# Kernel tuning notes

Hardware: AMD Instinct MI355X
Metric: run time of the kernel (lower is better)

Reference implementation:

```python
import jax, jax.numpy as jnp
import numpy as np
from jax import lax

B, C_IN, C_OUT, H, W, E = 16, 256, 256, 32, 32, 8


def setup_inputs() -> dict:
    key = jax.random.key(0)
    k = jax.random.split(key, 5)
    x = jax.random.normal(k[0], (B, C_IN, H, W), dtype=jnp.float32)
    # router: Conv2d(C_IN, E, kernel_size=1) -> weight [E, C_IN], bias [E]
    wc = jax.random.normal(k[1], (E, C_IN), dtype=jnp.float32) / np.sqrt(C_IN)
    bc = jnp.zeros((E,), dtype=jnp.float32)
    # experts: E x Conv2d(C_IN, C_OUT, 3, padding=1) + ReLU
    we = jax.random.normal(k[2], (E, C_OUT, C_IN, 3, 3), dtype=jnp.float32) / np.sqrt(C_IN * 9)
    be = jnp.zeros((E, C_OUT), dtype=jnp.float32)
    return {"x": x, "wc": wc, "bc": bc, "we": we, "be": be}


def reference(x, wc, bc, we, be):
    Bx = x.shape[0]
    # controller: 1x1 conv then global avg-pool == pool then linear
    pooled = jnp.mean(x, axis=(2, 3))                      # [B, C_IN]
    logits = pooled @ wc.T + bc                            # [B, E]
    decisions = jnp.argmax(logits, axis=1)                 # [B] int
    # run ALL experts on the full batch as one grouped conv: weight [E*C_OUT, C_IN, 3, 3]
    w_all = we.reshape(E * C_OUT, C_IN, 3, 3)
    y = lax.conv_general_dilated(
        x, w_all, window_strides=(1, 1), padding="SAME",
        dimension_numbers=("NCHW", "OIHW", "NCHW"))        # [B, E*C_OUT, H, W]
    y = y + be.reshape(1, E * C_OUT, 1, 1)
    y = jax.nn.relu(y).reshape(Bx, E, C_OUT, H, W)
    # faithful to forward_test: out block i is components[dec[i]](x) for the FULL batch
    # out[i*B + j] = y[j, dec[i]]
    gathered = y[:, decisions]                             # [j, i, C_OUT, H, W]
    out = jnp.swapaxes(gathered, 0, 1).reshape(Bx * Bx, C_OUT, H, W)
    return out
```

## Files before the change

### kernel.cpp

```cpp
#include <hip/hip_runtime.h>
#include <hip/hip_bf16.h>
#include <stdint.h>

#define B_    16
#define CIN   256
#define COUT  256
#define E_    8
#define HW    1024
#define PH    34
#define PW    34

typedef __attribute__((ext_vector_type(8))) short  short8;
typedef __attribute__((ext_vector_type(4))) float  floatx4;

#define XT_OFF 17408
#define XT_BYTES (B_*PH*PW*CIN*2)
#define WT_OFF (XT_OFF + XT_BYTES)

__device__ __forceinline__ void gld_lds16(const void* g, void* l) {
    __builtin_amdgcn_global_load_lds(
        (const __attribute__((address_space(1))) unsigned int*)g,
        (__attribute__((address_space(3))) unsigned int*)l,
        16, 0, 0);
}

__global__ void pool_kernel(const float* __restrict__ x, float* __restrict__ pooled) {
    int b = blockIdx.x, c = blockIdx.y;
    const float4* p = (const float4*)(x + ((size_t)b*CIN + c)*HW);
    int t = threadIdx.x;
    float4 v = p[t];
    float s = v.x + v.y + v.z + v.w;
    #pragma unroll
    for (int o = 32; o > 0; o >>= 1) s += __shfl_down(s, o, 64);
    __shared__ float wsum[4];
    if ((t & 63) == 0) wsum[t >> 6] = s;
    __syncthreads();
    if (t == 0) pooled[b*CIN + c] = (wsum[0]+wsum[1]+wsum[2]+wsum[3]) * (1.0f/1024.0f);
}

__global__ void decide_kernel(const float* __restrict__ pooled, const float* __restrict__ wc,
                              const float* __restrict__ bc, int* __restrict__ dec) {
    int t = threadIdx.x;
    int b = t >> 3, e = t & 7;
    float acc = bc[e];
    const float4* pp = (const float4*)(pooled + b*CIN);
    const float4* ww = (const float4*)(wc + e*CIN);
    #pragma unroll 4
    for (int i = 0; i < CIN/4; ++i) {
        float4 p = pp[i], w = ww[i];
        acc += p.x*w.x + p.y*w.y + p.z*w.z + p.w*w.w;
    }
    __shared__ float lg[16][8];
    lg[b][e] = acc;
    __syncthreads();
    if (e == 0) {
        float best = lg[b][0]; int bi = 0;
        #pragma unroll
        for (int j = 1; j < 8; ++j) { if (lg[b][j] > best) { best = lg[b][j]; bi = j; } }
        dec[b] = bi;
    }
}

__global__ void xpose_kernel(const float* __restrict__ x, unsigned short* __restrict__ xt) {
    int b = blockIdx.x;
    int hw0 = blockIdx.y * 32;
    int ci0 = blockIdx.z * 32;
    __shared__ float tile[32][33];
    int t = threadIdx.x;
    int j = t & 31;
    int i = t >> 5;
    #pragma unroll
    for (int p = 0; p < 4; ++p)
        tile[i + p*8][j] = x[((size_t)b*CIN + ci0 + i + p*8)*HW + hw0 + j];
    __syncthreads();
    if (t < 128) {
        int g = t & 3;
        int hwl = t >> 2;
        int hw = hw0 + hwl;
        int h = hw >> 5, w = hw & 31;
        short8 v;
        #pragma unroll
        for (int q = 0; q < 8; ++q) {
            __hip_bfloat16 hv = __float2bfloat16(tile[g*8 + q][hwl]);
            v[q] = *(short*)&hv;
        }
        *(short8*)&xt[(((size_t)b*PH + h + 1)*PW + (w + 1))*CIN + ci0 + g*8] = v;
    }
}

__global__ void wpose_kernel(const float* __restrict__ we, unsigned short* __restrict__ wt) {
    int e = blockIdx.x >> 8, co = blockIdx.x & 255;
    __shared__ float buf[CIN*9];
    const float* src = we + ((size_t)e*COUT + co)*CIN*9;
    int t = threadIdx.x;
    #pragma unroll
    for (int k = 0; k < 9; ++k) buf[t + k*256] = src[t + k*256];
    __syncthreads();
    for (int idx = t; idx < 288; idx += 256) {
        int rs = idx >> 5, grp = idx & 31;
        short8 v;
        #pragma unroll
        for (int q = 0; q < 8; ++q) {
            __hip_bfloat16 h = __float2bfloat16(buf[(grp*8 + q)*9 + rs]);
            v[q] = *(short*)&h;
        }
        *(short8*)&wt[(((size_t)e*9 + rs)*COUT + co)*CIN + grp*8] = v;
    }
}

__global__ __launch_bounds__(256) void conv_kernel(
    const unsigned short* __restrict__ xt, const unsigned short* __restrict__ wt,
    const float* __restrict__ be, const int* __restrict__ dec,
    float* __restrict__ out) {

    int tile = blockIdx.x;
    int b = blockIdx.y;
    int e = blockIdx.z;
    int mt = tile >> 3, nt = tile & 7;

    int dcs[16];
    #pragma unroll
    for (int i = 0; i < 16; ++i) dcs[i] = dec[i];
    bool active = false;
    #pragma unroll
    for (int i = 0; i < 16; ++i) active |= (dcs[i] == e);
    if (!active) return;

    __shared__ __align__(16) unsigned short sA[3][512*8];
    __shared__ __align__(16) unsigned short sB[2][832*8];

    int t = threadIdx.x;
    int wave = t >> 6, lane = t & 63;
    int wm = wave >> 1, wn = wave & 1;
    int kg = lane >> 4, ln = lane & 15;

    int ph0 = nt * 4;
    int co0 = mt * 128;

    floatx4 acc[4][4];
    #pragma unroll
    for (int i = 0; i < 4; ++i)
        #pragma unroll
        for (int j = 0; j < 4; ++j) acc[i][j] = (floatx4)0.0f;

    const unsigned short* xb = xt + ((size_t)b*PH + ph0)*PW*CIN;
    const unsigned short* wb = wt + (size_t)e*9*COUT*CIN + (size_t)co0*CIN;

    auto stageA = [&](int ck, int sh, int buf) {
        const unsigned short* wsrc = wb + (size_t)sh*COUT*CIN + ck*32;
        #pragma unroll
        for (int k = 0; k < 2; ++k) {
            int c = t + k*256;
            int row = c >> 2, gs = c & 3;
            int g = gs ^ ((row >> 1) & 3);
            gld_lds16(wsrc + (size_t)row*CIN + g*8, &sA[buf][c*8]);
        }
    };
    auto stageB = [&](int ck, int buf) {
        const unsigned short* xsrc = xb + ck*32;
        #pragma unroll
        for (int k = 0; k < 3; ++k) {
            int c = t + k*256;
            int rB = c >> 2, gs = c & 3;
            int g = gs ^ ((rB >> 1) & 3);
            gld_lds16(xsrc + (size_t)rB*CIN + g*8, &sB[buf][c*8]);
        }
        if (t < 64) {
            int c = t + 768;
            int cc = c < 816 ? c : 815;
            int rB = cc >> 2, gs = cc & 3;
            int g = gs ^ ((rB >> 1) & 3);
            gld_lds16(xsrc + (size_t)rB*CIN + g*8, &sB[buf][c*8]);
        }
    };

    stageB(0, 0);
    stageA(0, 0, 0);
    stageA(0, 1, 1);
    asm volatile("s_waitcnt vmcnt(2)" ::: "memory");
    __builtin_amdgcn_s_barrier();

    for (int ck = 0; ck < 8; ++ck) {
        int bb_ = ck & 1;
        for (int sh = 0; sh < 9; ++sh) {
            int it = ck*9 + sh;
            int ab = it % 3;

            int nit = it + 2;
            bool doA = (nit < 72);
            if (doA) {
                int nck = nit / 9;
                stageA(nck, nit - nck*9, nit % 3);
            }
            bool doB = (sh == 7) && (ck < 7);
            if (doB) stageB(ck + 1, bb_ ^ 1);

            short8 a[4], bv[4];
            #pragma unroll
            for (int im = 0; im < 4; ++im) {
                int row = wm*64 + im*16 + ln;
                int cL = row*4 + (kg ^ ((row >> 1) & 3));
                a[im] = *(const short8*)(&sA[ab][cL*8]);
            }
            int r = sh / 3, s = sh - r*3;
            #pragma unroll
            for (int in = 0; in < 4; ++in) {
                int n  = wn*64 + in*16 + ln;
                int hl = n >> 5, wl = n & 31;
                int rB = (hl + r)*34 + (wl + s);
                int cL = rB*4 + (kg ^ ((rB >> 1) & 3));
                bv[in] = *(const short8*)(&sB[bb_][cL*8]);
            }

            #pragma unroll
            for (int im = 0; im < 4; ++im)
                #pragma unroll
                for (int in = 0; in < 4; ++in)
                    acc[im][in] = __builtin_amdgcn_mfma_f32_16x16x32_bf16(bv[in], a[im], acc[im][in], 0, 0, 0);

            if (doA) {
                if (doB) {
                    if (wave == 0) asm volatile("s_waitcnt vmcnt(6) lgkmcnt(0)" ::: "memory");
                    else           asm volatile("s_waitcnt vmcnt(5) lgkmcnt(0)" ::: "memory");
                } else {
                    asm volatile("s_waitcnt vmcnt(2) lgkmcnt(0)" ::: "memory");
                }
            } else {
                asm volatile("s_waitcnt vmcnt(0) lgkmcnt(0)" ::: "memory");
            }
            __builtin_amdgcn_s_barrier();
        }
    }

    float bias[4];
    #pragma unroll
    for (int im = 0; im < 4; ++im)
        bias[im] = be[e*COUT + co0 + wm*64 + im*16 + ln];
    #pragma unroll
    for (int im = 0; im < 4; ++im)
        #pragma unroll
        for (int in = 0; in < 4; ++in)
            #pragma unroll
            for (int rg = 0; rg < 4; ++rg) {
                float v = acc[im][in][rg] + bias[im];
                acc[im][in][rg] = v > 0.0f ? v : 0.0f;
            }

    for (int i = 0; i < 16; ++i) {
        if (dcs[i] != e) continue;
        float* ob = out + (size_t)(i*16 + b)*COUT*HW;
        #pragma unroll
        for (int im = 0; im < 4; ++im) {
            int co = co0 + wm*64 + im*16 + ln;
            float* orow = ob + (size_t)co*HW + nt*128 + wn*64 + kg*4;
            #pragma unroll
            for (int in = 0; in < 4; ++in)
                *(floatx4*)(orow + in*16) = acc[im][in];
        }
    }
}

extern "C" void kernel_launch(void* const* d_in, const int* in_sizes, int n_in,
                              void* d_out, int out_size, void* d_ws, size_t ws_size,
                              hipStream_t stream) {
    const float* x  = (const float*)d_in[0];
    const float* wc = (const float*)d_in[1];
    const float* bc = (const float*)d_in[2];
    const float* we = (const float*)d_in[3];
    const float* be = (const float*)d_in[4];
    float* out = (float*)d_out;

    char* ws = (char*)d_ws;
    int*   dec    = (int*)ws;
    float* pooled = (float*)(ws + 64);
    unsigned short* xt = (unsigned short*)(ws + XT_OFF);
    unsigned short* wt = (unsigned short*)(ws + WT_OFF);

    hipMemsetAsync(xt, 0, XT_BYTES, stream);

    pool_kernel  <<<dim3(16, 256), 256, 0, stream>>>(x, pooled);
    decide_kernel<<<1, 128, 0, stream>>>(pooled, wc, bc, dec);
    xpose_kernel <<<dim3(16, 32, 8), 256, 0, stream>>>(x, xt);
    wpose_kernel <<<2048, 256, 0, stream>>>(we, wt);
    conv_kernel  <<<dim3(16, 16, 8), 256, 0, stream>>>(xt, wt, be, dec, out);
}
```

Measured before the change: 453.6 us.

## Fuse pooling into transpose and single-buffer conv input tile for occupancy

Folds the global average pool into the input transpose kernel with per-tile sums accumulated through atomicAdd, which removes a separate pass over x. The 1/1024 scale moves into the decision kernel, and the memset now also zeroes the pooled buffer. The conv kernel drops the double-buffered input tile to a single buffer, reloading it after a barrier at the last shift of each channel chunk, and adds a launch bound of 4 blocks per CU. The aim is to cut LDS use and raise occupancy, at the cost of an extra barrier and load stall once per chunk.

```diff
diff --git a/kernel.cpp b/kernel.cpp
--- a/kernel.cpp
+++ b/kernel.cpp
@@ -24,25 +24,45 @@
         16, 0, 0);
 }
 
-__global__ void pool_kernel(const float* __restrict__ x, float* __restrict__ pooled) {
-    int b = blockIdx.x, c = blockIdx.y;
-    const float4* p = (const float4*)(x + ((size_t)b*CIN + c)*HW);
-    int t = threadIdx.x;
-    float4 v = p[t];
-    float s = v.x + v.y + v.z + v.w;
-    #pragma unroll
-    for (int o = 32; o > 0; o >>= 1) s += __shfl_down(s, o, 64);
-    __shared__ float wsum[4];
-    if ((t & 63) == 0) wsum[t >> 6] = s;
+__global__ void xpose_kernel(const float* __restrict__ x, unsigned short* __restrict__ xt,
+                             float* __restrict__ pooled) {
+    int b = blockIdx.x;
+    int hw0 = blockIdx.y * 32;
+    int ci0 = blockIdx.z * 32;
+    __shared__ float tile[32][33];
+    int t = threadIdx.x;
+    int j = t & 31;
+    int i = t >> 5;
+    #pragma unroll
+    for (int p = 0; p < 4; ++p)
+        tile[i + p*8][j] = x[((size_t)b*CIN + ci0 + i + p*8)*HW + hw0 + j];
     __syncthreads();
-    if (t == 0) pooled[b*CIN + c] = (wsum[0]+wsum[1]+wsum[2]+wsum[3]) * (1.0f/1024.0f);
+    if (t < 32) {
+        float s = 0.0f;
+        #pragma unroll
+        for (int q = 0; q < 32; ++q) s += tile[t][q];
+        atomicAdd(&pooled[b*CIN + ci0 + t], s);
+    }
+    if (t < 128) {
+        int g = t & 3;
+        int hwl = t >> 2;
+        int hw = hw0 + hwl;
+        int h = hw >> 5, w = hw & 31;
+        short8 v;
+        #pragma unroll
+        for (int q = 0; q < 8; ++q) {
+            __hip_bfloat16 hv = __float2bfloat16(tile[g*8 + q][hwl]);
+            v[q] = *(short*)&hv;
+        }
+        *(short8*)&xt[(((size_t)b*PH + h + 1)*PW + (w + 1))*CIN + ci0 + g*8] = v;
+    }
 }
 
 __global__ void decide_kernel(const float* __restrict__ pooled, const float* __restrict__ wc,
                               const float* __restrict__ bc, int* __restrict__ dec) {
     int t = threadIdx.x;
     int b = t >> 3, e = t & 7;
-    float acc = bc[e];
+    float acc = 0.0f;
     const float4* pp = (const float4*)(pooled + b*CIN);
     const float4* ww = (const float4*)(wc + e*CIN);
     #pragma unroll 4
@@ -50,6 +70,7 @@
         float4 p = pp[i], w = ww[i];
         acc += p.x*w.x + p.y*w.y + p.z*w.z + p.w*w.w;
     }
+    acc = acc * (1.0f/1024.0f) + bc[e];
     __shared__ float lg[16][8];
     lg[b][e] = acc;
     __syncthreads();
@@ -61,33 +82,6 @@
     }
 }
 
-__global__ void xpose_kernel(const float* __restrict__ x, unsigned short* __restrict__ xt) {
-    int b = blockIdx.x;
-    int hw0 = blockIdx.y * 32;
-    int ci0 = blockIdx.z * 32;
-    __shared__ float tile[32][33];
-    int t = threadIdx.x;
-    int j = t & 31;
-    int i = t >> 5;
-    #pragma unroll
-    for (int p = 0; p < 4; ++p)
-        tile[i + p*8][j] = x[((size_t)b*CIN + ci0 + i + p*8)*HW + hw0 + j];
-    __syncthreads();
-    if (t < 128) {
-        int g = t & 3;
-        int hwl = t >> 2;
-        int hw = hw0 + hwl;
-        int h = hw >> 5, w = hw & 31;
-        short8 v;
-        #pragma unroll
-        for (int q = 0; q < 8; ++q) {
-            __hip_bfloat16 hv = __float2bfloat16(tile[g*8 + q][hwl]);
-            v[q] = *(short*)&hv;
-        }
-        *(short8*)&xt[(((size_t)b*PH + h + 1)*PW + (w + 1))*CIN + ci0 + g*8] = v;
-    }
-}
-
 __global__ void wpose_kernel(const float* __restrict__ we, unsigned short* __restrict__ wt) {
     int e = blockIdx.x >> 8, co = blockIdx.x & 255;
     __shared__ float buf[CIN*9];
@@ -108,7 +102,7 @@
     }
 }
 
-__global__ __launch_bounds__(256) void conv_kernel(
+__global__ __launch_bounds__(256, 4) void conv_kernel(
     const unsigned short* __restrict__ xt, const unsigned short* __restrict__ wt,
     const float* __restrict__ be, const int* __restrict__ dec,
     float* __restrict__ out) {
@@ -127,7 +121,7 @@
     if (!active) return;
 
     __shared__ __align__(16) unsigned short sA[3][512*8];
-    __shared__ __align__(16) unsigned short sB[2][832*8];
+    __shared__ __align__(16) unsigned short sB[816*8];
 
     int t = threadIdx.x;
     int wave = t >> 6, lane = t & 63;
@@ -156,60 +150,69 @@
             gld_lds16(wsrc + (size_t)row*CIN + g*8, &sA[buf][c*8]);
         }
     };
-    auto stageB = [&](int ck, int buf) {
+    auto stageB = [&](int ck) {
         const unsigned short* xsrc = xb + ck*32;
         #pragma unroll
         for (int k = 0; k < 3; ++k) {
             int c = t + k*256;
             int rB = c >> 2, gs = c & 3;
             int g = gs ^ ((rB >> 1) & 3);
-            gld_lds16(xsrc + (size_t)rB*CIN + g*8, &sB[buf][c*8]);
+            gld_lds16(xsrc + (size_t)rB*CIN + g*8, &sB[c*8]);
         }
         if (t < 64) {
             int c = t + 768;
             int cc = c < 816 ? c : 815;
             int rB = cc >> 2, gs = cc & 3;
             int g = gs ^ ((rB >> 1) & 3);
-            gld_lds16(xsrc + (size_t)rB*CIN + g*8, &sB[buf][c*8]);
+            if (c < 816) gld_lds16(xsrc + (size_t)rB*CIN + g*8, &sB[c*8]);
+            else         gld_lds16(xsrc + (size_t)rB*CIN + g*8, &sB[815*8]);
         }
     };
 
-    stageB(0, 0);
+    stageB(0);
     stageA(0, 0, 0);
     stageA(0, 1, 1);
     asm volatile("s_waitcnt vmcnt(2)" ::: "memory");
     __builtin_amdgcn_s_barrier();
 
     for (int ck = 0; ck < 8; ++ck) {
-        int bb_ = ck & 1;
         for (int sh = 0; sh < 9; ++sh) {
             int it = ck*9 + sh;
             int ab = it % 3;
-
-            int nit = it + 2;
-            bool doA = (nit < 72);
-            if (doA) {
-                int nck = nit / 9;
-                stageA(nck, nit - nck*9, nit % 3);
-            }
-            bool doB = (sh == 7) && (ck < 7);
-            if (doB) stageB(ck + 1, bb_ ^ 1);
+            int r = sh / 3, s = sh - r*3;
+            bool doA = (it + 2 < 72);
 
             short8 a[4], bv[4];
-            #pragma unroll
-            for (int im = 0; im < 4; ++im) {
-                int row = wm*64 + im*16 + ln;
-                int cL = row*4 + (kg ^ ((row >> 1) & 3));
-                a[im] = *(const short8*)(&sA[ab][cL*8]);
-            }
-            int r = sh / 3, s = sh - r*3;
-            #pragma unroll
-            for (int in = 0; in < 4; ++in) {
-                int n  = wn*64 + in*16 + ln;
-                int hl = n >> 5, wl = n & 31;
-                int rB = (hl + r)*34 + (wl + s);
-                int cL = rB*4 + (kg ^ ((rB >> 1) & 3));
-                bv[in] = *(const short8*)(&sB[bb_][cL*8]);
+            auto readA = [&]() {
+                #pragma unroll
+                for (int im = 0; im < 4; ++im) {
+                    int row = wm*64 + im*16 + ln;
+                    int cL = row*4 + (kg ^ ((row >> 1) & 3));
+                    a[im] = *(const short8*)(&sA[ab][cL*8]);
+                }
+            };
+            auto readB = [&]() {
+                #pragma unroll
+                for (int in = 0; in < 4; ++in) {
+                    int n  = wn*64 + in*16 + ln;
+                    int hl = n >> 5, wl = n & 31;
+                    int rB = (hl + r)*34 + (wl + s);
+                    int cL = rB*4 + (kg ^ ((rB >> 1) & 3));
+                    bv[in] = *(const short8*)(&sB[cL*8]);
+                }
+            };
+
+            if (sh == 8 && ck < 7) {
+                readB();
+                asm volatile("s_waitcnt lgkmcnt(0)" ::: "memory");
+                __builtin_amdgcn_s_barrier();
+                stageB(ck + 1);
+                { int nit = it + 2; int nck = nit/9; stageA(nck, nit - nck*9, nit % 3); }
+                readA();
+            } else {
+                if (doA) { int nit = it + 2; int nck = nit/9; stageA(nck, nit - nck*9, nit % 3); }
+                readA();
+                readB();
             }
 
             #pragma unroll
@@ -218,17 +221,11 @@
                 for (int in = 0; in < 4; ++in)
                     acc[im][in] = __builtin_amdgcn_mfma_f32_16x16x32_bf16(bv[in], a[im], acc[im][in], 0, 0, 0);
 
-            if (doA) {
-                if (doB) {
-                    if (wave == 0) asm volatile("s_waitcnt vmcnt(6) lgkmcnt(0)" ::: "memory");
-                    else           asm volatile("s_waitcnt vmcnt(5) lgkmcnt(0)" ::: "memory");
-                } else {
-                    asm volatile("s_waitcnt vmcnt(2) lgkmcnt(0)" ::: "memory");
-                }
-            } else {
-                asm volatile("s_waitcnt vmcnt(0) lgkmcnt(0)" ::: "memory");
+            if (it != 71) {
+                if (doA) asm volatile("s_waitcnt vmcnt(2) lgkmcnt(0)" ::: "memory");
+                else     asm volatile("s_waitcnt vmcnt(0) lgkmcnt(0)" ::: "memory");
+                __builtin_amdgcn_s_barrier();
             }
-            __builtin_amdgcn_s_barrier();
         }
     }
 
@@ -276,11 +273,10 @@
     unsigned short* xt = (unsigned short*)(ws + XT_OFF);
     unsigned short* wt = (unsigned short*)(ws + WT_OFF);
 
-    hipMemsetAsync(xt, 0, XT_BYTES, stream);
-
-    pool_kernel  <<<dim3(16, 256), 256, 0, stream>>>(x, pooled);
+    hipMemsetAsync(ws, 0, XT_OFF + XT_BYTES, stream);
+
+    xpose_kernel <<<dim3(16, 32, 8), 256, 0, stream>>>(x, xt, pooled);
+    wpose_kernel <<<2048, 256, 0, stream>>>(we, wt);
     decide_kernel<<<1, 128, 0, stream>>>(pooled, wc, bc, dec);
-    xpose_kernel <<<dim3(16, 32, 8), 256, 0, stream>>>(x, xt);
-    wpose_kernel <<<2048, 256, 0, stream>>>(we, wt);
     conv_kernel  <<<dim3(16, 16, 8), 256, 0, stream>>>(xt, wt, be, dec, out);
 }
```

Result: slower. 491.4 us (+8.3%).

## Fuse prep kernels, compute routing inside conv, simplify pipeline to double buffering

Applied to the files above, without the earlier changes.

Merges pooling, activation transpose, border zeroing and weight transpose into one prep kernel, which removes the full-tensor memset and several launches. Each conv block now recomputes the router logits and argmax from the pooled sums, so the separate decide kernel goes away. The conv main loop drops the triple-buffered A pipeline with hand-tuned vmcnt waits in favour of plain double buffering with __syncthreads, which may expose more load latency. sB grows to 1024 rows, so LDS use per block rises.

```diff
diff --git a/kernel.cpp b/kernel.cpp
--- a/kernel.cpp
+++ b/kernel.cpp
@@ -24,112 +24,122 @@
         16, 0, 0);
 }
 
-__global__ void pool_kernel(const float* __restrict__ x, float* __restrict__ pooled) {
-    int b = blockIdx.x, c = blockIdx.y;
-    const float4* p = (const float4*)(x + ((size_t)b*CIN + c)*HW);
+__global__ void prep_kernel(const float* __restrict__ x, const float* __restrict__ we,
+                            unsigned short* __restrict__ xt, unsigned short* __restrict__ wt,
+                            float* __restrict__ pooled) {
+    int bid = blockIdx.x;
     int t = threadIdx.x;
-    float4 v = p[t];
-    float s = v.x + v.y + v.z + v.w;
-    #pragma unroll
-    for (int o = 32; o > 0; o >>= 1) s += __shfl_down(s, o, 64);
-    __shared__ float wsum[4];
-    if ((t & 63) == 0) wsum[t >> 6] = s;
-    __syncthreads();
-    if (t == 0) pooled[b*CIN + c] = (wsum[0]+wsum[1]+wsum[2]+wsum[3]) * (1.0f/1024.0f);
-}
-
-__global__ void decide_kernel(const float* __restrict__ pooled, const float* __restrict__ wc,
-                              const float* __restrict__ bc, int* __restrict__ dec) {
-    int t = threadIdx.x;
-    int b = t >> 3, e = t & 7;
-    float acc = bc[e];
-    const float4* pp = (const float4*)(pooled + b*CIN);
-    const float4* ww = (const float4*)(wc + e*CIN);
-    #pragma unroll 4
-    for (int i = 0; i < CIN/4; ++i) {
-        float4 p = pp[i], w = ww[i];
-        acc += p.x*w.x + p.y*w.y + p.z*w.z + p.w*w.w;
-    }
-    __shared__ float lg[16][8];
-    lg[b][e] = acc;
-    __syncthreads();
-    if (e == 0) {
-        float best = lg[b][0]; int bi = 0;
-        #pragma unroll
-        for (int j = 1; j < 8; ++j) { if (lg[b][j] > best) { best = lg[b][j]; bi = j; } }
-        dec[b] = bi;
-    }
-}
-
-__global__ void xpose_kernel(const float* __restrict__ x, unsigned short* __restrict__ xt) {
-    int b = blockIdx.x;
-    int hw0 = blockIdx.y * 32;
-    int ci0 = blockIdx.z * 32;
-    __shared__ float tile[32][33];
-    int t = threadIdx.x;
-    int j = t & 31;
-    int i = t >> 5;
-    #pragma unroll
-    for (int p = 0; p < 4; ++p)
-        tile[i + p*8][j] = x[((size_t)b*CIN + ci0 + i + p*8)*HW + hw0 + j];
-    __syncthreads();
-    if (t < 128) {
-        int g = t & 3;
-        int hwl = t >> 2;
-        int hw = hw0 + hwl;
-        int h = hw >> 5, w = hw & 31;
-        short8 v;
-        #pragma unroll
-        for (int q = 0; q < 8; ++q) {
-            __hip_bfloat16 hv = __float2bfloat16(tile[g*8 + q][hwl]);
-            v[q] = *(short*)&hv;
-        }
-        *(short8*)&xt[(((size_t)b*PH + h + 1)*PW + (w + 1))*CIN + ci0 + g*8] = v;
-    }
-}
-
-__global__ void wpose_kernel(const float* __restrict__ we, unsigned short* __restrict__ wt) {
-    int e = blockIdx.x >> 8, co = blockIdx.x & 255;
-    __shared__ float buf[CIN*9];
-    const float* src = we + ((size_t)e*COUT + co)*CIN*9;
-    int t = threadIdx.x;
-    #pragma unroll
-    for (int k = 0; k < 9; ++k) buf[t + k*256] = src[t + k*256];
-    __syncthreads();
-    for (int idx = t; idx < 288; idx += 256) {
-        int rs = idx >> 5, grp = idx & 31;
-        short8 v;
-        #pragma unroll
-        for (int q = 0; q < 8; ++q) {
-            __hip_bfloat16 h = __float2bfloat16(buf[(grp*8 + q)*9 + rs]);
-            v[q] = *(short*)&h;
-        }
-        *(short8*)&wt[(((size_t)e*9 + rs)*COUT + co)*CIN + grp*8] = v;
+    if (bid < 128) {
+        int b = bid >> 3, ci0 = (bid & 7) * 32;
+        __shared__ float tileF[32][65];
+        float psum[8];
+        #pragma unroll
+        for (int li = 0; li < 8; ++li) psum[li] = 0.0f;
+        int hwl = t & 63, wv = t >> 6;
+        int hwl2 = t >> 2, grp = t & 3;
+        for (int chunk = 0; chunk < 16; ++chunk) {
+            #pragma unroll
+            for (int li = 0; li < 8; ++li) {
+                int ci = wv + li*4;
+                float v = x[((size_t)b*CIN + ci0 + ci)*HW + chunk*64 + hwl];
+                tileF[ci][hwl] = v;
+                psum[li] += v;
+            }
+            __syncthreads();
+            int hw = chunk*64 + hwl2;
+            int h = hw >> 5, w = hw & 31;
+            short8 v8;
+            #pragma unroll
+            for (int q = 0; q < 8; ++q) {
+                __hip_bfloat16 hv = __float2bfloat16(tileF[grp*8 + q][hwl2]);
+                v8[q] = *(short*)&hv;
+            }
+            *(short8*)&xt[(((size_t)b*PH + h + 1)*PW + (w + 1))*CIN + ci0 + grp*8] = v8;
+            __syncthreads();
+        }
+        #pragma unroll
+        for (int li = 0; li < 8; ++li) {
+            float s = psum[li];
+            #pragma unroll
+            for (int o = 32; o > 0; o >>= 1) s += __shfl_down(s, o, 64);
+            if ((t & 63) == 0) pooled[b*CIN + ci0 + wv + li*4] = s;
+        }
+        short8 z = {0,0,0,0,0,0,0,0};
+        for (int idx = t; idx < 528; idx += 256) {
+            int pos = idx >> 2, sub = idx & 3;
+            int h, w;
+            if (pos < 34)       { h = 0;            w = pos; }
+            else if (pos < 68)  { h = 33;           w = pos - 34; }
+            else if (pos < 100) { h = pos - 68 + 1; w = 0; }
+            else                { h = pos - 100 + 1;w = 33; }
+            *(short8*)&xt[(((size_t)b*PH + h)*PW + w)*CIN + ci0 + sub*8] = z;
+        }
+    } else {
+        int wbid = bid - 128;
+        int e = wbid >> 8, co = wbid & 255;
+        __shared__ float buf[CIN*9];
+        const float* src = we + ((size_t)e*COUT + co)*CIN*9;
+        #pragma unroll
+        for (int k = 0; k < 9; ++k) buf[t + k*256] = src[t + k*256];
+        __syncthreads();
+        for (int idx = t; idx < 288; idx += 256) {
+            int rs = idx >> 5, grp = idx & 31;
+            short8 v;
+            #pragma unroll
+            for (int q = 0; q < 8; ++q) {
+                __hip_bfloat16 h = __float2bfloat16(buf[(grp*8 + q)*9 + rs]);
+                v[q] = *(short*)&h;
+            }
+            *(short8*)&wt[(((size_t)e*9 + rs)*COUT + co)*CIN + grp*8] = v;
+        }
     }
 }
 
 __global__ __launch_bounds__(256) void conv_kernel(
     const unsigned short* __restrict__ xt, const unsigned short* __restrict__ wt,
-    const float* __restrict__ be, const int* __restrict__ dec,
+    const float* __restrict__ pooled, const float* __restrict__ wc,
+    const float* __restrict__ bc, const float* __restrict__ be,
     float* __restrict__ out) {
 
     int tile = blockIdx.x;
     int b = blockIdx.y;
     int e = blockIdx.z;
     int mt = tile >> 3, nt = tile & 7;
-
+    int t = threadIdx.x;
+
+    __shared__ float lg[16][8];
+    __shared__ int sdec[16];
+    if (t < 128) {
+        int bb = t >> 3, ee = t & 7;
+        float acc = 0.0f;
+        const float4* pp = (const float4*)(pooled + bb*CIN);
+        const float4* ww = (const float4*)(wc + ee*CIN);
+        #pragma unroll 4
+        for (int i = 0; i < CIN/4; ++i) {
+            float4 p = pp[i], w = ww[i];
+            acc += p.x*w.x + p.y*w.y + p.z*w.z + p.w*w.w;
+        }
+        lg[bb][ee] = acc * (1.0f/1024.0f) + bc[ee];
+    }
+    __syncthreads();
+    if (t < 16) {
+        float best = lg[t][0]; int bi = 0;
+        #pragma unroll
+        for (int j = 1; j < 8; ++j) if (lg[t][j] > best) { best = lg[t][j]; bi = j; }
+        sdec[t] = bi;
+    }
+    __syncthreads();
     int dcs[16];
     #pragma unroll
-    for (int i = 0; i < 16; ++i) dcs[i] = dec[i];
+    for (int i = 0; i < 16; ++i) dcs[i] = sdec[i];
     bool active = false;
     #pragma unroll
     for (int i = 0; i < 16; ++i) active |= (dcs[i] == e);
     if (!active) return;
 
-    __shared__ __align__(16) unsigned short sA[3][512*8];
-    __shared__ __align__(16) unsigned short sB[2][832*8];
-
-    int t = threadIdx.x;
+    __shared__ __align__(16) unsigned short sA[2][512*8];
+    __shared__ __align__(16) unsigned short sB[2][1024*8];
+
     int wave = t >> 6, lane = t & 63;
     int wm = wave >> 1, wn = wave & 1;
     int kg = lane >> 4, ln = lane & 15;
@@ -176,24 +186,19 @@
 
     stageB(0, 0);
     stageA(0, 0, 0);
-    stageA(0, 1, 1);
-    asm volatile("s_waitcnt vmcnt(2)" ::: "memory");
-    __builtin_amdgcn_s_barrier();
+    __syncthreads();
 
     for (int ck = 0; ck < 8; ++ck) {
-        int bb_ = ck & 1;
         for (int sh = 0; sh < 9; ++sh) {
             int it = ck*9 + sh;
-            int ab = it % 3;
-
-            int nit = it + 2;
-            bool doA = (nit < 72);
-            if (doA) {
-                int nck = nit / 9;
-                stageA(nck, nit - nck*9, nit % 3);
-            }
-            bool doB = (sh == 7) && (ck < 7);
-            if (doB) stageB(ck + 1, bb_ ^ 1);
+            int ab = it & 1, bb_ = ck & 1;
+
+            if (sh < 8) {
+                stageA(ck, sh + 1, ab ^ 1);
+            } else if (ck < 7) {
+                stageA(ck + 1, 0, ab ^ 1);
+                stageB(ck + 1, bb_ ^ 1);
+            }
 
             short8 a[4], bv[4];
             #pragma unroll
@@ -218,17 +223,7 @@
                 for (int in = 0; in < 4; ++in)
                     acc[im][in] = __builtin_amdgcn_mfma_f32_16x16x32_bf16(bv[in], a[im], acc[im][in], 0, 0, 0);
 
-            if (doA) {
-                if (doB) {
-                    if (wave == 0) asm volatile("s_waitcnt vmcnt(6) lgkmcnt(0)" ::: "memory");
-                    else           asm volatile("s_waitcnt vmcnt(5) lgkmcnt(0)" ::: "memory");
-                } else {
-                    asm volatile("s_waitcnt vmcnt(2) lgkmcnt(0)" ::: "memory");
-                }
-            } else {
-                asm volatile("s_waitcnt vmcnt(0) lgkmcnt(0)" ::: "memory");
-            }
-            __builtin_amdgcn_s_barrier();
+            __syncthreads();
         }
     }
 
@@ -271,16 +266,10 @@
     float* out = (float*)d_out;
 
     char* ws = (char*)d_ws;
-    int*   dec    = (int*)ws;
     float* pooled = (float*)(ws + 64);
     unsigned short* xt = (unsigned short*)(ws + XT_OFF);
     unsigned short* wt = (unsigned short*)(ws + WT_OFF);
 
-    hipMemsetAsync(xt, 0, XT_BYTES, stream);
-
-    pool_kernel  <<<dim3(16, 256), 256, 0, stream>>>(x, pooled);
-    decide_kernel<<<1, 128, 0, stream>>>(pooled, wc, bc, dec);
-    xpose_kernel <<<dim3(16, 32, 8), 256, 0, stream>>>(x, xt);
-    wpose_kernel <<<2048, 256, 0, stream>>>(we, wt);
-    conv_kernel  <<<dim3(16, 16, 8), 256, 0, stream>>>(xt, wt, be, dec, out);
-}
+    prep_kernel<<<2176, 256, 0, stream>>>(x, we, xt, wt, pooled);
+    conv_kernel<<<dim3(16, 16, 8), 256, 0, stream>>>(xt, wt, pooled, wc, bc, be, out);
+}
```

New measurement: 481.4 us. 1.06x slower.
